# Performance work log

Hardware: AMD Instinct MI355X
Metric: run time of the kernel (lower is better)

The kernel has to match this reference:

```python
import jax, jax.numpy as jnp
import numpy as np

# dims: C=d_model, DI=expand*C (d_inner), S=d_state, R=dt_rank, K=4 scan dirs
C, DI, S, R, K = 64, 128, 16, 4, 4
Hh, Ww, T, Bsz = 48, 48, 4, 1

def _silu(x):
    return x * jax.nn.sigmoid(x)

def _ln_c(x, w, b, eps=1e-6):
    # LayerNorm2d: normalize over channel dim of [B,C,H,W]
    mu = jnp.mean(x, axis=1, keepdims=True)
    var = jnp.var(x, axis=1, keepdims=True)
    return (x - mu) * jax.lax.rsqrt(var + eps) * w[None, :, None, None] + b[None, :, None, None]

def _cal_kl(cur, prev):
    # elementwise KL over channel-softmax distributions, shape-preserving
    lp = jax.nn.log_softmax(prev, axis=1)
    lq = jax.nn.log_softmax(cur, axis=1)
    return jnp.exp(lp) * (lp - lq)

def _ss2d(x, in_w, in_b, cw, cb, xp_w, dt_w, dt_b, A_logs, Ds, onw, onb, ow, ob):
    # VMamba-style SS2D, channel-first input [B,C,H,W]
    B_, _, H_, W_ = x.shape
    L = H_ * W_
    xz = jnp.einsum('dc,bchw->bdhw', in_w, x) + in_b[None, :, None, None]
    xc, z = jnp.split(xz, 2, axis=1)
    di = xc.shape[1]
    xc = jax.lax.conv_general_dilated(xc, cw[:, None], (1, 1), 'SAME',
        dimension_numbers=('NCHW', 'OIHW', 'NCHW'), feature_group_count=di)
    xc = _silu(xc + cb[None, :, None, None])
    # cross-scan: row-major, col-major, and their reverses -> [B,K,DI,L]
    x1 = xc.reshape(B_, di, L)
    x2 = jnp.swapaxes(xc, 2, 3).reshape(B_, di, L)
    xs = jnp.stack([x1, x2, jnp.flip(x1, -1), jnp.flip(x2, -1)], axis=1)
    xdbl = jnp.einsum('krd,bkdl->bkrl', xp_w, xs)
    dts, Bs, Cs = jnp.split(xdbl, [R, R + S], axis=2)  # [B,K,R,L],[B,K,S,L],[B,K,S,L]
    dt = jax.nn.softplus(jnp.einsum('kdr,bkrl->bkdl', dt_w, dts) + dt_b[None, :, :, None])
    A = -jnp.exp(A_logs)  # [K,DI,S]
    dA = jnp.exp(dt[..., None] * A[None, :, :, None, :])                    # [B,K,DI,L,S]
    dBx = (dt * xs)[..., None] * jnp.swapaxes(Bs, 2, 3)[:, :, None, :, :]   # [B,K,DI,L,S]
    def comb(e1, e2):
        a1, b1 = e1
        a2, b2 = e2
        return (a1 * a2, a2 * b1 + b2)
    _, hs = jax.lax.associative_scan(comb, (dA, dBx), axis=3)
    y = jnp.einsum('bkdls,bksl->bkdl', hs, Cs) + Ds[None, :, :, None] * xs
    # cross-merge back to row-major and sum
    y0 = y[:, 0]
    y1 = jnp.swapaxes(y[:, 1].reshape(B_, di, W_, H_), 2, 3).reshape(B_, di, L)
    y2 = jnp.flip(y[:, 2], -1)
    y3 = jnp.swapaxes(jnp.flip(y[:, 3], -1).reshape(B_, di, W_, H_), 2, 3).reshape(B_, di, L)
    yy = (y0 + y1 + y2 + y3).reshape(B_, di, H_, W_)
    yy = _ln_c(yy, onw, onb) * _silu(z)
    return jnp.einsum('cd,bdhw->bchw', ow, yy) + ob[None, :, None, None]

def setup_inputs():
    key = jax.random.key(0)
    ks = jax.random.split(key, 16)
    rn = lambda k, shp, s: jax.random.normal(k, shp, jnp.float32) * s
    return {
        'image_sequence': rn(ks[0], (Bsz, T, C, Hh, Ww), 1.0),
        'difficult_zone': rn(ks[1], (Bsz, C, Hh, Ww), 1.0),
        'sigma': rn(ks[2], (Bsz, C, Hh, Ww), 0.1),
        # params stacked over the 2 SS2D modules: [0]=mamba_sigma, [1]=mamba_bias
        'in_w': rn(ks[3], (2, 2 * DI, C), C ** -0.5),
        'in_b': rn(ks[4], (2, 2 * DI), 0.02),
        'conv_w': rn(ks[5], (2, DI, 3, 3), 1.0 / 3.0),
        'conv_b': rn(ks[6], (2, DI), 0.02),
        'xp_w': rn(ks[7], (2, K, R + 2 * S, DI), DI ** -0.5),
        'dt_w': rn(ks[8], (2, K, DI, R), R ** -0.5),
        'dt_b': rn(ks[9], (2, K, DI), 0.5),
        'A_logs': jnp.log(1.0 + jax.random.uniform(ks[10], (2, K, DI, S), jnp.float32)),
        'Ds': rn(ks[11], (2, K, DI), 0.5),
        'onw': jnp.ones((2, DI), jnp.float32),
        'onb': jnp.zeros((2, DI), jnp.float32),
        'ow': rn(ks[12], (2, C, DI), 0.02),
        'ob': jnp.zeros((2, C), jnp.float32),
        'niw': jnp.ones((C,), jnp.float32),
        'nib': jnp.zeros((C,), jnp.float32),
        'ndw': jnp.ones((C,), jnp.float32),
        'ndb': jnp.zeros((C,), jnp.float32),
    }

def reference(image_sequence, difficult_zone, sigma, in_w, in_b, conv_w, conv_b, xp_w, dt_w, dt_b, A_logs, Ds, onw, onb, ow, ob, niw, nib, ndw, ndb):
    prev = _ln_c(difficult_zone, ndw, ndb)
    cur = prev * jnp.exp(sigma)  # prev / exp(-sigma)
    for t in range(T):  # strictly sequential recurrence over `length` steps
        s = _ss2d(_cal_kl(cur, prev), in_w[0], in_b[0], conv_w[0], conv_b[0], xp_w[0],
                  dt_w[0], dt_b[0], A_logs[0], Ds[0], onw[0], onb[0], ow[0], ob[0])
        bias = _ss2d(_ln_c(image_sequence[:, t], niw, nib), in_w[1], in_b[1], conv_w[1], conv_b[1], xp_w[1],
                     dt_w[1], dt_b[1], A_logs[1], Ds[1], onw[1], onb[1], ow[1], ob[1])
        cur, prev = cur * jnp.exp(s) + bias, cur
    return cur
```

## Files before the change

kernel.cpp:

```cpp
#include <hip/hip_runtime.h>

#define DEV __device__ __forceinline__

constexpr int Cc = 64, DIc = 128, Sc = 16, Rc = 4, Kc = 4;
constexpr int Lc = 2304, Tc = 4;
constexpr int NCH = 144, CHL = 16;

constexpr int OFF_XCPRE = 0;
constexpr int OFF_Z     = 294912;
constexpr int OFF_XACT  = 589824;
constexpr int OFF_DTS   = 884736;
constexpr int OFF_BS    = 921600;
constexpr int OFF_CS    = 1069056;
constexpr int OFF_Y     = 1216512;
constexpr int OFF_SUMA  = 2396160;
constexpr int OFF_SUMB  = 3575808;
constexpr int OFF_H0    = 4755456;
constexpr int SLOTF     = 5935104;
constexpr int OFF_B1    = 5 * SLOTF;
constexpr int OFF_B2    = OFF_B1 + Lc * Cc;
constexpr int OFF_BIAS  = OFF_B2 + Lc * Cc;
constexpr int OFF_TW    = OFF_BIAS + Tc * Lc * Cc;
constexpr int TW_INW  = 0;
constexpr int TW_XPW  = 32768;
constexpr int TW_OW   = 69632;
constexpr int TW_CW   = 86016;
constexpr int TW_AT   = 88320;
constexpr int TW_DTW  = 104704;

struct Params {
  const float *img, *dz, *sigma, *in_w, *in_b, *conv_w, *conv_b, *xp_w, *dt_w,
              *dt_b, *A_logs, *Ds, *onw, *onb, *ow, *ob, *niw, *nib, *ndw, *ndb;
  float* outp;
  float* ws;
};

DEV float wsum(float v) {
#pragma unroll
  for (int m = 32; m; m >>= 1) v += __shfl_xor(v, m, 64);
  return v;
}
DEV float wmax(float v) {
#pragma unroll
  for (int m = 32; m; m >>= 1) v = fmaxf(v, __shfl_xor(v, m, 64));
  return v;
}
DEV float sigmoidf(float x) { return 1.f / (1.f + __expf(-x)); }
DEV float softplusf(float v) { return (v > 20.f) ? v : __logf(1.f + __expf(v)); }
DEV float fexp2(float x) { return __builtin_amdgcn_exp2f(x); }

DEV int perm_idx(int k, int l) {
  if (k == 0) return l;
  if (k == 1) return (l % 48) * 48 + l / 48;
  if (k == 2) return Lc - 1 - l;
  int pp = Lc - 1 - l;
  return (pp % 48) * 48 + pp / 48;
}

DEV int perm_stride(int k) {
  return (k == 0) ? 1 : (k == 1) ? 48 : (k == 2) ? -1 : -48;
}

__global__ __launch_bounds__(256) void g_transpose(Params p) {
  float* tw = p.ws + OFF_TW;
  int i = blockIdx.x * 256 + threadIdx.x;
  if (i < 32768) {
    int d = i & 255, cc = (i >> 8) & 63, b = i >> 14;
    tw[TW_INW + i] = p.in_w[(b * 256 + d) * 64 + cc];
  }
  if (i < 36864) {
    int kr = i % 144, cc = (i / 144) & 127, b = i / (144 * 128);
    tw[TW_XPW + i] = p.xp_w[(b * 144 + kr) * 128 + cc];
  }
  if (i < 16384) {
    int c = i & 63, d = (i >> 6) & 127, b = i >> 13;
    tw[TW_OW + i] = p.ow[(b * 64 + c) * 128 + d];
  }
  if (i < 2304) {
    int d = i & 127, kk = (i >> 7) % 9, b = i / 1152;
    tw[TW_CW + i] = p.conv_w[(b * 128 + d) * 9 + kk];
  }
  if (i < 16384) {
    int d = i & 127, bks = i >> 7;
    int s = bks & 15, bk = bks >> 4;
    tw[TW_AT + i] = -__expf(p.A_logs[(bk * 128 + d) * 16 + s]) * 1.4426950408889634f;
  }
  if (i < 4096) {
    int d = i & 127, bkr = i >> 7;
    int r = bkr & 3, bk = bkr >> 2;
    tw[TW_DTW + i] = p.dt_w[(bk * 128 + d) * 4 + r];
  }
}

__global__ __launch_bounds__(256) void g_inproj(Params p) {
  __shared__ float xv[8][64];
  int tid = threadIdx.x;
  int slot = blockIdx.y;
  int branch = (slot >= 4) ? 0 : 1;
  float* ws = p.ws;
  float* base = ws + (size_t)slot * SLOTF;
  float* xcpre = base + OFF_XCPRE;
  float* zbuf  = base + OFF_Z;
  const float* wT = ws + OFF_TW + TW_INW + branch * 64 * 256;
  int l0 = blockIdx.x * 8;
  int wv = tid >> 6, c = tid & 63;
#pragma unroll
  for (int q = 0; q < 2; q++) {
    int pp = wv * 2 + q;
    int l = l0 + pp;
    float x;
    if (branch == 1) {
      float v = p.img[(slot * Cc + c) * Lc + l];
      float mu = wsum(v) * (1.f / 64.f);
      float var = wsum(v * v) * (1.f / 64.f) - mu * mu;
      x = (v - mu) * rsqrtf(var + 1e-6f) * p.niw[c] + p.nib[c];
    } else {
      float v = p.dz[c * Lc + l];
      float mu = wsum(v) * (1.f / 64.f);
      float var = wsum(v * v) * (1.f / 64.f) - mu * mu;
      float pv = (v - mu) * rsqrtf(var + 1e-6f) * p.ndw[c] + p.ndb[c];
      float cv = pv * __expf(p.sigma[c * Lc + l]);
      (ws + OFF_B1)[l * Cc + c] = cv;
      float mp = wmax(pv);
      float sp = wsum(__expf(pv - mp));
      float lp = pv - mp - __logf(sp);
      float mq = wmax(cv);
      float sq = wsum(__expf(cv - mq));
      float lq = cv - mq - __logf(sq);
      x = __expf(lp) * (lp - lq);
    }
    xv[pp][c] = x;
  }
  __syncthreads();
  int d = tid;
  float acc[8];
#pragma unroll
  for (int q = 0; q < 8; q++) acc[q] = 0.f;
  for (int cc = 0; cc < Cc; cc++) {
    float wval = wT[cc * 256 + d];
#pragma unroll
    for (int q = 0; q < 8; q++) acc[q] += wval * xv[q][cc];
  }
  float bv = p.in_b[branch * 2 * DIc + d];
  if (d < DIc) {
#pragma unroll
    for (int q = 0; q < 8; q++) xcpre[(l0 + q) * DIc + d] = acc[q] + bv;
  } else {
    int dd = d - DIc;
#pragma unroll
    for (int q = 0; q < 8; q++) zbuf[(l0 + q) * DIc + dd] = acc[q] + bv;
  }
}

__global__ __launch_bounds__(256) void g_conv(Params p, int slot_base) {
  __shared__ float xv[4][DIc];
  int tid = threadIdx.x;
  int slot = slot_base + blockIdx.y;
  int branch = (slot >= 4) ? 0 : 1;
  float* ws = p.ws;
  float* base = ws + (size_t)slot * SLOTF;
  float* xcpre = base + OFF_XCPRE;
  float* xact  = base + OFF_XACT;
  float* dtsb  = base + OFF_DTS;
  float* Bsb   = base + OFF_BS;
  float* Csb   = base + OFF_CS;
  const float* cwT  = ws + OFF_TW + TW_CW + branch * 9 * 128;
  const float* xpwT = ws + OFF_TW + TW_XPW + branch * 128 * 144;
  int h = blockIdx.x / 12;
  int w0 = (blockIdx.x % 12) * 4;
  for (int it = tid; it < 4 * DIc; it += 256) {
    int d = it & (DIc - 1);
    int pp = it >> 7;
    int w = w0 + pp;
    float acc = 0.f;
#pragma unroll
    for (int kh = 0; kh < 3; kh++) {
      int hh = h + kh - 1;
      if ((unsigned)hh < 48u) {
#pragma unroll
        for (int kw = 0; kw < 3; kw++) {
          int wp = w + kw - 1;
          if ((unsigned)wp < 48u)
            acc += cwT[(kh * 3 + kw) * 128 + d] * xcpre[(hh * 48 + wp) * DIc + d];
        }
      }
    }
    float v = acc + p.conv_b[branch * DIc + d];
    float s = v * sigmoidf(v);
    xv[pp][d] = s;
    xact[(h * 48 + w) * DIc + d] = s;
  }
  __syncthreads();
  if (tid < Kc * 36) {
    int k = tid / 36, r = tid % 36;
    float acc[4] = {0.f, 0.f, 0.f, 0.f};
    for (int cc = 0; cc < DIc; cc++) {
      float wvv = xpwT[cc * 144 + tid];
#pragma unroll
      for (int pp = 0; pp < 4; pp++) acc[pp] += wvv * xv[pp][cc];
    }
#pragma unroll
    for (int pp = 0; pp < 4; pp++) {
      int w = w0 + pp;
      int lr = h * 48 + w, lcx = w * 48 + h;
      int pos = (k == 0) ? lr : (k == 1) ? lcx : (k == 2) ? (Lc - 1 - lr) : (Lc - 1 - lcx);
      if (r < Rc) dtsb[(k * Lc + pos) * Rc + r] = acc[pp];
      else if (r < Rc + Sc) Bsb[(k * Lc + pos) * Sc + (r - Rc)] = acc[pp];
      else Csb[(k * Lc + pos) * Sc + (r - Rc - Sc)] = acc[pp];
    }
  }
}

__global__ __launch_bounds__(256, 4) void g_scan1(Params p, int slot_base) {
  __shared__ alignas(16) float sB[CHL * Sc];
  int tid = threadIdx.x;
  int slot = slot_base + blockIdx.y;
  int branch = (slot >= 4) ? 0 : 1;
  float* ws = p.ws;
  float* base = ws + (size_t)slot * SLOTF;
  const float* xact = base + OFF_XACT;
  const float* Bsb  = base + OFF_BS;
  const float* dtsb = base + OFF_DTS;
  float* sumA = base + OFF_SUMA;
  float* sumB = base + OFF_SUMB;
  int bx = blockIdx.x;
  int k = bx / NCH, ch = bx - k * NCH;
  int d = tid & (DIc - 1);
  int sh = tid >> 7;
  int bk = branch * Kc + k;
  const float* AT   = ws + OFF_TW + TW_AT;
  const float* dtwT = ws + OFF_TW + TW_DTW;
  int l0 = ch * CHL;
  sB[tid] = Bsb[(k * Lc + l0) * Sc + tid];
  float A2[8];
#pragma unroll
  for (int j = 0; j < 8; j++) A2[j] = AT[(bk * 16 + sh * 8 + j) * 128 + d];
  float dw0 = dtwT[(bk * 4 + 0) * 128 + d];
  float dw1 = dtwT[(bk * 4 + 1) * 128 + d];
  float dw2 = dtwT[(bk * 4 + 2) * 128 + d];
  float dw3 = dtwT[(bk * 4 + 3) * 128 + d];
  float db = p.dt_b[bk * DIc + d];
  int idx0 = perm_idx(k, l0);
  int st = perm_stride(k);
  float dtv[CHL], dtx[CHL];
  float CT = 0.f;
#pragma unroll
  for (int i = 0; i < CHL; i++) {
    float4 dt4 = *(const float4*)(dtsb + (size_t)(k * Lc + l0 + i) * 4);
    float v = db + dw0 * dt4.x + dw1 * dt4.y + dw2 * dt4.z + dw3 * dt4.w;
    float t = softplusf(v);
    dtv[i] = t;
    dtx[i] = t * xact[(idx0 + st * i) * DIc + d];
    CT += t;
  }
  __syncthreads();
  const float4* B4 = (const float4*)sB;
  float h[8];
#pragma unroll
  for (int j = 0; j < 8; j++) h[j] = 0.f;
#pragma unroll
  for (int i = 0; i < CHL; i++) {
    float4 Bg0 = B4[i * 4 + sh * 2];
    float4 Bg1 = B4[i * 4 + sh * 2 + 1];
    float t = dtv[i], tx = dtx[i];
#define STEP1(hh, bb, aa2) { float da = fexp2(t * (aa2)); hh = da * hh + tx * (bb); }
    STEP1(h[0], Bg0.x, A2[0]);
    STEP1(h[1], Bg0.y, A2[1]);
    STEP1(h[2], Bg0.z, A2[2]);
    STEP1(h[3], Bg0.w, A2[3]);
    STEP1(h[4], Bg1.x, A2[4]);
    STEP1(h[5], Bg1.y, A2[5]);
    STEP1(h[6], Bg1.z, A2[6]);
    STEP1(h[7], Bg1.w, A2[7]);
#undef STEP1
  }
  float* sa = sumA + ((size_t)(k * NCH + ch) * Sc + sh * 8) * DIc + d;
  float* sb = sumB + ((size_t)(k * NCH + ch) * Sc + sh * 8) * DIc + d;
#pragma unroll
  for (int j = 0; j < 8; j++) sa[j * DIc] = fexp2(A2[j] * CT);
#pragma unroll
  for (int j = 0; j < 8; j++) sb[j * DIc] = h[j];
}

__global__ __launch_bounds__(256) void g_mid(Params p, int slot_base) {
  int gid = blockIdx.x * 256 + threadIdx.x;
  int slot = slot_base + blockIdx.y;
  float* base = p.ws + (size_t)slot * SLOTF;
  const float* sumA = base + OFF_SUMA;
  const float* sumB = base + OFF_SUMB;
  float* h0 = base + OFF_H0;
  int d = gid & (DIc - 1);
  int s = (gid >> 7) & (Sc - 1);
  int k = gid >> 11;
  float h = 0.f;
  for (int g = 0; g < NCH / 16; g++) {
    float a[16], b[16];
#pragma unroll
    for (int j = 0; j < 16; j++) {
      int idx = ((k * NCH + g * 16 + j) * Sc + s) * DIc + d;
      a[j] = sumA[idx];
      b[j] = sumB[idx];
    }
#pragma unroll
    for (int j = 0; j < 16; j++) {
      int idx = ((k * NCH + g * 16 + j) * Sc + s) * DIc + d;
      h0[idx] = h;
      h = a[j] * h + b[j];
    }
  }
}

__global__ __launch_bounds__(256, 4) void g_scan2(Params p, int slot_base) {
  __shared__ alignas(16) float sB[2][CHL * Sc];
  __shared__ alignas(16) float sC[2][CHL * Sc];
  __shared__ alignas(16) float yred[2][CHL][64];
  int tid = threadIdx.x;
  int slot = slot_base + blockIdx.y;
  int branch = (slot >= 4) ? 0 : 1;
  float* ws = p.ws;
  float* base = ws + (size_t)slot * SLOTF;
  const float* xact = base + OFF_XACT;
  const float* Bsb  = base + OFF_BS;
  const float* Csb  = base + OFF_CS;
  const float* dtsb = base + OFF_DTS;
  const float* h0b  = base + OFF_H0;
  int bx = blockIdx.x;
  int pair = bx / (2 * NCH);
  int rem = bx - pair * 2 * NCH;
  int chA = rem >> 1;
  int dblk = rem & 1;
  int dm = tid & 63;
  int d = dblk * 64 + dm;
  int sh = (tid >> 6) & 1;
  int dir = tid >> 7;
  int kA = pair, kB = pair + 2;
  int l0A = chA * CHL, l0B = (NCH - 1 - chA) * CHL;
  sB[0][tid] = Bsb[(kA * Lc + l0A) * Sc + tid];
  sB[1][tid] = Bsb[(kB * Lc + l0B) * Sc + tid];
  sC[0][tid] = Csb[(kA * Lc + l0A) * Sc + tid];
  sC[1][tid] = Csb[(kB * Lc + l0B) * Sc + tid];
  int k = dir ? kB : kA;
  int ch = dir ? (NCH - 1 - chA) : chA;
  int bk = branch * Kc + k;
  float* ypair = base + OFF_Y + (size_t)pair * Lc * DIc;
  const float* AT   = ws + OFF_TW + TW_AT;
  const float* dtwT = ws + OFF_TW + TW_DTW;
  int l0 = ch * CHL;
  float A2[8];
#pragma unroll
  for (int j = 0; j < 8; j++) A2[j] = AT[(bk * 16 + sh * 8 + j) * 128 + d];
  float h[8];
  {
    const float* hp = h0b + ((size_t)(k * NCH + ch) * Sc + sh * 8) * DIc + d;
#pragma unroll
    for (int j = 0; j < 8; j++) h[j] = hp[j * DIc];
  }
  float dw0 = dtwT[(bk * 4 + 0) * 128 + d];
  float dw1 = dtwT[(bk * 4 + 1) * 128 + d];
  float dw2 = dtwT[(bk * 4 + 2) * 128 + d];
  float dw3 = dtwT[(bk * 4 + 3) * 128 + d];
  float db = p.dt_b[bk * DIc + d];
  float Dv = p.Ds[bk * DIc + d];
  int idx0 = perm_idx(k, l0);
  int st = perm_stride(k);
  float dtv[CHL], dtx[CHL], acc[CHL];
#pragma unroll
  for (int i = 0; i < CHL; i++) {
    float4 dt4 = *(const float4*)(dtsb + (size_t)(k * Lc + l0 + i) * 4);
    float v = db + dw0 * dt4.x + dw1 * dt4.y + dw2 * dt4.z + dw3 * dt4.w;
    float t = softplusf(v);
    float xv = xact[(idx0 + st * i) * DIc + d];
    dtv[i] = t;
    dtx[i] = t * xv;
    acc[i] = (sh == 0) ? Dv * xv : 0.f;
  }
  __syncthreads();
  const float4* B4 = (const float4*)sB[dir];
  const float4* C4 = (const float4*)sC[dir];
#pragma unroll
  for (int i = 0; i < CHL; i++) {
    float4 Bg0 = B4[i * 4 + sh * 2];
    float4 Bg1 = B4[i * 4 + sh * 2 + 1];
    float4 Cg0 = C4[i * 4 + sh * 2];
    float4 Cg1 = C4[i * 4 + sh * 2 + 1];
    float t = dtv[i], tx = dtx[i];
    float a = acc[i];
#define STEP(hh, bb, cc, aa2) { float da = fexp2(t * (aa2)); hh = da * hh + tx * (bb); a += hh * (cc); }
    STEP(h[0], Bg0.x, Cg0.x, A2[0]);
    STEP(h[1], Bg0.y, Cg0.y, A2[1]);
    STEP(h[2], Bg0.z, Cg0.z, A2[2]);
    STEP(h[3], Bg0.w, Cg0.w, A2[3]);
    STEP(h[4], Bg1.x, Cg1.x, A2[4]);
    STEP(h[5], Bg1.y, Cg1.y, A2[5]);
    STEP(h[6], Bg1.z, Cg1.z, A2[6]);
    STEP(h[7], Bg1.w, Cg1.w, A2[7]);
#undef STEP
    acc[i] = a;
  }
  if (sh == 1) {
#pragma unroll
    for (int i = 0; i < CHL; i++) yred[dir][i][dm] = acc[i];
  }
  __syncthreads();
  if (sh == 0) {
#pragma unroll
    for (int i = 0; i < CHL; i++) yred[dir][i][dm] += acc[i];
  }
  __syncthreads();
  if (sh == 0 && dir == 0) {
#pragma unroll
    for (int i = 0; i < CHL; i++)
      ypair[(size_t)(idx0 + st * i) * DIc + d] =
          yred[0][i][dm] + yred[1][CHL - 1 - i][dm];
  }
}

__global__ __launch_bounds__(256) void g_out_bias(Params p) {
  __shared__ float yy[4][DIc];
  __shared__ float ml[4][DIc];
  __shared__ float mnv[4], isv[4];
  int tid = threadIdx.x;
  int slot = blockIdx.y;
  float* ws = p.ws;
  float* base = ws + (size_t)slot * SLOTF;
  const float* y01 = base + OFF_Y;
  const float* y23 = base + OFF_Y + Lc * DIc;
  const float* zb = base + OFF_Z;
  const float* owT = ws + OFF_TW + TW_OW + 128 * 64;
  float* biasb = ws + OFF_BIAS;
  int l0 = blockIdx.x * 4;
  for (int it = tid; it < 4 * DIc; it += 256) {
    int d = it & (DIc - 1), pp = it >> 7;
    size_t off = (size_t)(l0 + pp) * DIc + d;
    yy[pp][d] = y01[off] + y23[off];
  }
  __syncthreads();
  {
    int wv = tid >> 6, c = tid & 63;
    float a = yy[wv][c], b = yy[wv][c + 64];
    float s1 = wsum(a + b);
    float s2 = wsum(a * a + b * b);
    float mu = s1 * (1.f / 128.f);
    float var = s2 * (1.f / 128.f) - mu * mu;
    if (c == 0) { mnv[wv] = mu; isv[wv] = rsqrtf(var + 1e-6f); }
  }
  __syncthreads();
  for (int it = tid; it < 4 * DIc; it += 256) {
    int d = it & (DIc - 1), pp = it >> 7;
    int l = l0 + pp;
    float m = (yy[pp][d] - mnv[pp]) * isv[pp] * p.onw[DIc + d] + p.onb[DIc + d];
    float zv = zb[l * DIc + d];
    ml[pp][d] = m * zv * sigmoidf(zv);
  }
  __syncthreads();
  {
    int pp = tid >> 6, c = tid & 63;
    int l = l0 + pp;
    float acc = p.ob[Cc + c];
    for (int d2 = 0; d2 < DIc; d2++) acc += owT[d2 * 64 + c] * ml[pp][d2];
    biasb[(slot * Lc + l) * Cc + c] = acc;
  }
}

__global__ __launch_bounds__(256) void g_out_s(Params p, int targ, int fuse, int finalw,
                                               const float* curb, float* nxtb) {
  __shared__ float yy[4][DIc];
  __shared__ float ml[4][DIc];
  __shared__ float xvs[4][64];
  __shared__ float mnv[4], isv[4];
  int tid = threadIdx.x;
  float* ws = p.ws;
  float* base = ws + (size_t)4 * SLOTF;
  const float* y01 = base + OFF_Y;
  const float* y23 = base + OFF_Y + Lc * DIc;
  const float* zb = base + OFF_Z;
  float* xcpre = base + OFF_XCPRE;
  float* zbuf  = base + OFF_Z;
  const float* owT  = ws + OFF_TW + TW_OW;
  const float* inwT = ws + OFF_TW + TW_INW;
  const float* biasb = ws + OFF_BIAS;
  int l0 = blockIdx.x * 4;
  for (int it = tid; it < 4 * DIc; it += 256) {
    int d = it & (DIc - 1), pp = it >> 7;
    size_t off = (size_t)(l0 + pp) * DIc + d;
    yy[pp][d] = y01[off] + y23[off];
  }
  __syncthreads();
  {
    int wv = tid >> 6, c = tid & 63;
    float a = yy[wv][c], b = yy[wv][c + 64];
    float s1 = wsum(a + b);
    float s2 = wsum(a * a + b * b);
    float mu = s1 * (1.f / 128.f);
    float var = s2 * (1.f / 128.f) - mu * mu;
    if (c == 0) { mnv[wv] = mu; isv[wv] = rsqrtf(var + 1e-6f); }
  }
  __syncthreads();
  for (int it = tid; it < 4 * DIc; it += 256) {
    int d = it & (DIc - 1), pp = it >> 7;
    int l = l0 + pp;
    float m = (yy[pp][d] - mnv[pp]) * isv[pp] * p.onw[d] + p.onb[d];
    float zv = zb[l * DIc + d];
    ml[pp][d] = m * zv * sigmoidf(zv);
  }
  __syncthreads();
  {
    int pp = tid >> 6, c = tid & 63;
    int l = l0 + pp;
    float acc = p.ob[c];
    for (int d2 = 0; d2 < DIc; d2++) acc += owT[d2 * 64 + c] * ml[pp][d2];
    float cv = curb[l * Cc + c];
    float nv = cv * __expf(acc) + biasb[(targ * Lc + l) * Cc + c];
    nxtb[l * Cc + c] = nv;
    if (finalw) p.outp[c * Lc + l] = nv;
    if (fuse) {
      float mp = wmax(cv);
      float sp = wsum(__expf(cv - mp));
      float lp = cv - mp - __logf(sp);
      float mq = wmax(nv);
      float sq = wsum(__expf(nv - mq));
      float lq = nv - mq - __logf(sq);
      xvs[pp][c] = __expf(lp) * (lp - lq);
    }
  }
  if (fuse) {
    __syncthreads();
    int d = tid;
    float acc[4] = {0.f, 0.f, 0.f, 0.f};
    for (int cc = 0; cc < Cc; cc++) {
      float wval = inwT[cc * 256 + d];
#pragma unroll
      for (int pp = 0; pp < 4; pp++) acc[pp] += wval * xvs[pp][cc];
    }
    float bv = p.in_b[d];
    if (d < DIc) {
#pragma unroll
      for (int pp = 0; pp < 4; pp++) xcpre[(l0 + pp) * DIc + d] = acc[pp] + bv;
    } else {
      int dd = d - DIc;
#pragma unroll
      for (int pp = 0; pp < 4; pp++) zbuf[(l0 + pp) * DIc + dd] = acc[pp] + bv;
    }
  }
}

extern "C" void kernel_launch(void* const* d_in, const int* in_sizes, int n_in,
                              void* d_out, int out_size, void* d_ws, size_t ws_size,
                              hipStream_t stream) {
  (void)in_sizes; (void)n_in; (void)out_size; (void)ws_size;
  Params p;
  p.img    = (const float*)d_in[0];
  p.dz     = (const float*)d_in[1];
  p.sigma  = (const float*)d_in[2];
  p.in_w   = (const float*)d_in[3];
  p.in_b   = (const float*)d_in[4];
  p.conv_w = (const float*)d_in[5];
  p.conv_b = (const float*)d_in[6];
  p.xp_w   = (const float*)d_in[7];
  p.dt_w   = (const float*)d_in[8];
  p.dt_b   = (const float*)d_in[9];
  p.A_logs = (const float*)d_in[10];
  p.Ds     = (const float*)d_in[11];
  p.onw    = (const float*)d_in[12];
  p.onb    = (const float*)d_in[13];
  p.ow     = (const float*)d_in[14];
  p.ob     = (const float*)d_in[15];
  p.niw    = (const float*)d_in[16];
  p.nib    = (const float*)d_in[17];
  p.ndw    = (const float*)d_in[18];
  p.ndb    = (const float*)d_in[19];
  p.outp   = (float*)d_out;
  p.ws     = (float*)d_ws;


  hipLaunchKernelGGL(g_transpose, dim3(144), dim3(256), 0, stream, p);
  hipLaunchKernelGGL(g_inproj, dim3(288, 5), dim3(256), 0, stream, p);
  hipLaunchKernelGGL(g_conv, dim3(576, 5), dim3(256), 0, stream, p, 0);
  hipLaunchKernelGGL(g_scan1, dim3(Kc * NCH, 5), dim3(256), 0, stream, p, 0);
  hipLaunchKernelGGL(g_mid, dim3(32, 5), dim3(256), 0, stream, p, 0);
  hipLaunchKernelGGL(g_scan2, dim3(2 * NCH * 2, 5), dim3(256), 0, stream, p, 0);
  hipLaunchKernelGGL(g_out_bias, dim3(576, 4), dim3(256), 0, stream, p);

  float* b1 = p.ws + OFF_B1;
  float* b2 = p.ws + OFF_B2;
  hipLaunchKernelGGL(g_out_s, dim3(576), dim3(256), 0, stream, p, 0, 1, 0,
                     (const float*)b1, b2);
  for (int t = 1; t < Tc; t++) {
    const float* curb = (t & 1) ? b2 : b1;
    float* nxtb       = (t & 1) ? b1 : b2;
    hipLaunchKernelGGL(g_conv, dim3(576, 1), dim3(256), 0, stream, p, 4);
    hipLaunchKernelGGL(g_scan1, dim3(Kc * NCH, 1), dim3(256), 0, stream, p, 4);
    hipLaunchKernelGGL(g_mid, dim3(32, 1), dim3(256), 0, stream, p, 4);
    hipLaunchKernelGGL(g_scan2, dim3(2 * NCH * 2, 1), dim3(256), 0, stream, p, 4);
    hipLaunchKernelGGL(g_out_s, dim3(576), dim3(256), 0, stream, p,
                       t, (t == Tc - 1) ? 0 : 1, (t == Tc - 1) ? 1 : 0, curb, nxtb);
  }
}
```

Measured before the change: 389.5 us.

## Split scan1 state dimension across blocks and parallelize chunk-carry scan in g_mid

g_scan1 now launches twice as many blocks, each handling 4 of the 16 state channels per thread instead of 8. This raises parallelism and lowers register pressure, but the per-chunk dt/softplus prologue is now recomputed twice. g_mid used to run 32 blocks whose threads each walked all 144 chunks serially. It now runs 256 blocks, splits the chunks into 8 groups of 18, and combines the group carries with a shared-memory Hillis-Steele scan before writing the starting states. The aim is to remove the long serial latency of the mid pass, at the cost of extra syncs and strided loads.

```diff
diff --git a/kernel.cpp b/kernel.cpp
--- a/kernel.cpp
+++ b/kernel.cpp
@@ -224,17 +224,20 @@
   float* sumA = base + OFF_SUMA;
   float* sumB = base + OFF_SUMB;
   int bx = blockIdx.x;
-  int k = bx / NCH, ch = bx - k * NCH;
+  int shb = bx & 1;
+  int kch = bx >> 1;
+  int k = kch / NCH, ch = kch - k * NCH;
   int d = tid & (DIc - 1);
-  int sh = tid >> 7;
+  int sq = tid >> 7;
+  int s0 = shb * 8 + sq * 4;
   int bk = branch * Kc + k;
   const float* AT   = ws + OFF_TW + TW_AT;
   const float* dtwT = ws + OFF_TW + TW_DTW;
   int l0 = ch * CHL;
   sB[tid] = Bsb[(k * Lc + l0) * Sc + tid];
-  float A2[8];
-#pragma unroll
-  for (int j = 0; j < 8; j++) A2[j] = AT[(bk * 16 + sh * 8 + j) * 128 + d];
+  float A2[4];
+#pragma unroll
+  for (int j = 0; j < 4; j++) A2[j] = AT[(bk * 16 + s0 + j) * 128 + d];
   float dw0 = dtwT[(bk * 4 + 0) * 128 + d];
   float dw1 = dtwT[(bk * 4 + 1) * 128 + d];
   float dw2 = dtwT[(bk * 4 + 2) * 128 + d];
@@ -255,58 +258,75 @@
   }
   __syncthreads();
   const float4* B4 = (const float4*)sB;
-  float h[8];
-#pragma unroll
-  for (int j = 0; j < 8; j++) h[j] = 0.f;
+  float h[4];
+#pragma unroll
+  for (int j = 0; j < 4; j++) h[j] = 0.f;
 #pragma unroll
   for (int i = 0; i < CHL; i++) {
-    float4 Bg0 = B4[i * 4 + sh * 2];
-    float4 Bg1 = B4[i * 4 + sh * 2 + 1];
+    float4 Bg = B4[i * 4 + (s0 >> 2)];
     float t = dtv[i], tx = dtx[i];
 #define STEP1(hh, bb, aa2) { float da = fexp2(t * (aa2)); hh = da * hh + tx * (bb); }
-    STEP1(h[0], Bg0.x, A2[0]);
-    STEP1(h[1], Bg0.y, A2[1]);
-    STEP1(h[2], Bg0.z, A2[2]);
-    STEP1(h[3], Bg0.w, A2[3]);
-    STEP1(h[4], Bg1.x, A2[4]);
-    STEP1(h[5], Bg1.y, A2[5]);
-    STEP1(h[6], Bg1.z, A2[6]);
-    STEP1(h[7], Bg1.w, A2[7]);
+    STEP1(h[0], Bg.x, A2[0]);
+    STEP1(h[1], Bg.y, A2[1]);
+    STEP1(h[2], Bg.z, A2[2]);
+    STEP1(h[3], Bg.w, A2[3]);
 #undef STEP1
   }
-  float* sa = sumA + ((size_t)(k * NCH + ch) * Sc + sh * 8) * DIc + d;
-  float* sb = sumB + ((size_t)(k * NCH + ch) * Sc + sh * 8) * DIc + d;
-#pragma unroll
-  for (int j = 0; j < 8; j++) sa[j * DIc] = fexp2(A2[j] * CT);
-#pragma unroll
-  for (int j = 0; j < 8; j++) sb[j * DIc] = h[j];
+  float* sa = sumA + ((size_t)(k * NCH + ch) * Sc + s0) * DIc + d;
+  float* sb = sumB + ((size_t)(k * NCH + ch) * Sc + s0) * DIc + d;
+#pragma unroll
+  for (int j = 0; j < 4; j++) sa[j * DIc] = fexp2(A2[j] * CT);
+#pragma unroll
+  for (int j = 0; j < 4; j++) sb[j * DIc] = h[j];
 }
 
 __global__ __launch_bounds__(256) void g_mid(Params p, int slot_base) {
-  int gid = blockIdx.x * 256 + threadIdx.x;
+  __shared__ float sA[8][33], sBs[8][33];
+  int tid = threadIdx.x;
   int slot = slot_base + blockIdx.y;
   float* base = p.ws + (size_t)slot * SLOTF;
   const float* sumA = base + OFF_SUMA;
   const float* sumB = base + OFF_SUMB;
   float* h0 = base + OFF_H0;
-  int d = gid & (DIc - 1);
-  int s = (gid >> 7) & (Sc - 1);
-  int k = gid >> 11;
-  float h = 0.f;
-  for (int g = 0; g < NCH / 16; g++) {
-    float a[16], b[16];
-#pragma unroll
-    for (int j = 0; j < 16; j++) {
-      int idx = ((k * NCH + g * 16 + j) * Sc + s) * DIc + d;
-      a[j] = sumA[idx];
-      b[j] = sumB[idx];
-    }
-#pragma unroll
-    for (int j = 0; j < 16; j++) {
-      int idx = ((k * NCH + g * 16 + j) * Sc + s) * DIc + d;
-      h0[idx] = h;
-      h = a[j] * h + b[j];
-    }
+  int bx = blockIdx.x;
+  int k = bx >> 6;
+  int s = (bx >> 2) & 15;
+  int dblk = bx & 3;
+  int dl = tid & 31;
+  int g = tid >> 5;
+  int d = dblk * 32 + dl;
+  float a[18], b[18];
+#pragma unroll
+  for (int j = 0; j < 18; j++) {
+    size_t idx = ((size_t)(k * NCH + g * 18 + j) * Sc + s) * DIc + d;
+    a[j] = sumA[idx];
+    b[j] = sumB[idx];
+  }
+  float Ag = 1.f, Bg = 0.f;
+#pragma unroll
+  for (int j = 0; j < 18; j++) { Bg = a[j] * Bg + b[j]; Ag *= a[j]; }
+  sA[g][dl] = Ag; sBs[g][dl] = Bg;
+  __syncthreads();
+  float Ai = Ag, Bi = Bg;
+#pragma unroll
+  for (int off = 1; off < 8; off <<= 1) {
+    float Ap = 1.f, Bp = 0.f;
+    bool take = (g >= off);
+    if (take) { Ap = sA[g - off][dl]; Bp = sBs[g - off][dl]; }
+    __syncthreads();
+    if (take) {
+      Bi = Ai * Bp + Bi;
+      Ai = Ai * Ap;
+      sA[g][dl] = Ai; sBs[g][dl] = Bi;
+    }
+    __syncthreads();
+  }
+  float h = (g == 0) ? 0.f : sBs[g - 1][dl];
+#pragma unroll
+  for (int j = 0; j < 18; j++) {
+    size_t idx = ((size_t)(k * NCH + g * 18 + j) * Sc + s) * DIc + d;
+    h0[idx] = h;
+    h = a[j] * h + b[j];
   }
 }
 
@@ -576,8 +596,8 @@
   hipLaunchKernelGGL(g_transpose, dim3(144), dim3(256), 0, stream, p);
   hipLaunchKernelGGL(g_inproj, dim3(288, 5), dim3(256), 0, stream, p);
   hipLaunchKernelGGL(g_conv, dim3(576, 5), dim3(256), 0, stream, p, 0);
-  hipLaunchKernelGGL(g_scan1, dim3(Kc * NCH, 5), dim3(256), 0, stream, p, 0);
-  hipLaunchKernelGGL(g_mid, dim3(32, 5), dim3(256), 0, stream, p, 0);
+  hipLaunchKernelGGL(g_scan1, dim3(Kc * NCH * 2, 5), dim3(256), 0, stream, p, 0);
+  hipLaunchKernelGGL(g_mid, dim3(256, 5), dim3(256), 0, stream, p, 0);
   hipLaunchKernelGGL(g_scan2, dim3(2 * NCH * 2, 5), dim3(256), 0, stream, p, 0);
   hipLaunchKernelGGL(g_out_bias, dim3(576, 4), dim3(256), 0, stream, p);
 
@@ -589,8 +609,8 @@
     const float* curb = (t & 1) ? b2 : b1;
     float* nxtb       = (t & 1) ? b1 : b2;
     hipLaunchKernelGGL(g_conv, dim3(576, 1), dim3(256), 0, stream, p, 4);
-    hipLaunchKernelGGL(g_scan1, dim3(Kc * NCH, 1), dim3(256), 0, stream, p, 4);
-    hipLaunchKernelGGL(g_mid, dim3(32, 1), dim3(256), 0, stream, p, 4);
+    hipLaunchKernelGGL(g_scan1, dim3(Kc * NCH * 2, 1), dim3(256), 0, stream, p, 4);
+    hipLaunchKernelGGL(g_mid, dim3(256, 1), dim3(256), 0, stream, p, 4);
     hipLaunchKernelGGL(g_scan2, dim3(2 * NCH * 2, 1), dim3(256), 0, stream, p, 4);
     hipLaunchKernelGGL(g_out_s, dim3(576), dim3(256), 0, stream, p,
                        t, (t == Tc - 1) ? 0 : 1, (t == Tc - 1) ? 1 : 0, curb, nxtb);
```

New measurement: 384.2 us, median of 2. Within noise of the previous version (-1.4%).
